# Kernel tuning notes

Measured on AMD Instinct MI355X. Metric: run time of the kernel, lower is better.

The kernel has to match this reference:

```python
import jax, jax.numpy as jnp
import numpy as np

D = 256; DFFN = 1024; H = 8; NLVL = 4; NPNT = 4; HD = D // H
BS = 4; NQ = 100; NPTS = 25
SPATIAL = [(128, 128), (64, 64), (32, 32), (16, 16)]
LEN_IN = sum(h * w for h, w in SPATIAL)


def _ln(x, g, b, eps=1e-5):
    m = x.mean(-1, keepdims=True)
    v = ((x - m) ** 2).mean(-1, keepdims=True)
    return (x - m) * jax.lax.rsqrt(v + eps) * g + b


def _mha(q, k, v, w_in, b_in, w_out, b_out):
    # torch nn.MultiheadAttention math, batch-first layout [B,S,D]
    B, Sq, _ = q.shape; Sk = k.shape[1]
    wq, wk, wv = jnp.split(w_in, 3, 0); bq, bk, bv = jnp.split(b_in, 3)
    qh = (q @ wq.T + bq).reshape(B, Sq, H, HD).transpose(0, 2, 1, 3)
    kh = (k @ wk.T + bk).reshape(B, Sk, H, HD).transpose(0, 2, 1, 3)
    vh = (v @ wv.T + bv).reshape(B, Sk, H, HD).transpose(0, 2, 1, 3)
    a = jax.nn.softmax(jnp.einsum('bhqd,bhkd->bhqk', qh, kh) * (1.0 / float(np.sqrt(HD))), -1)
    o = jnp.einsum('bhqk,bhkd->bhqd', a, vh).transpose(0, 2, 1, 3).reshape(B, Sq, D)
    return o @ w_out.T + b_out


def _msdeform(query, ref, src, off_w, off_b, aw_w, aw_b, val_w, val_b, out_w, out_b):
    # MSDeformAttn: per-query multi-level bilinear sampling + weighted aggregation
    bs, Lq, _ = query.shape
    value = (src @ val_w.T + val_b).reshape(bs, LEN_IN, H, HD)
    off = (query @ off_w.T + off_b).reshape(bs, Lq, H, NLVL, NPNT, 2)
    aw = jax.nn.softmax((query @ aw_w.T + aw_b).reshape(bs, Lq, H, NLVL * NPNT), -1)
    aw = aw.reshape(bs, Lq, H, NLVL, NPNT)
    norm = jnp.array([[w, h] for h, w in SPATIAL], jnp.float32)  # (W,H) per level
    loc = ref[:, :, None, :, None, :] + off / norm[None, None, None, :, None, :]
    out = jnp.zeros((bs, H, Lq, HD), query.dtype)
    start = 0
    for l, (hh, ww) in enumerate(SPATIAL):
        v_l = value[:, start:start + hh * ww].transpose(0, 2, 1, 3)  # [bs,H,hw,HD]
        start += hh * ww
        # grid_sample align_corners=False pixel coords: loc*size - 0.5
        x = (loc[:, :, :, l, :, 0] * ww - 0.5).transpose(0, 2, 1, 3).reshape(bs, H, Lq * NPNT)
        y = (loc[:, :, :, l, :, 1] * hh - 0.5).transpose(0, 2, 1, 3).reshape(bs, H, Lq * NPNT)
        x0 = jnp.floor(x); y0 = jnp.floor(y); wx = x - x0; wy = y - y0
        x0i = x0.astype(jnp.int32); y0i = y0.astype(jnp.int32); x1i = x0i + 1; y1i = y0i + 1
        def g(xi, yi):
            valid = ((xi >= 0) & (xi < ww) & (yi >= 0) & (yi < hh)).astype(query.dtype)
            idx = jnp.clip(yi, 0, hh - 1) * ww + jnp.clip(xi, 0, ww - 1)
            return jnp.take_along_axis(v_l, idx[..., None], axis=2) * valid[..., None]
        s = (g(x0i, y0i) * ((1 - wx) * (1 - wy))[..., None]
             + g(x1i, y0i) * (wx * (1 - wy))[..., None]
             + g(x0i, y1i) * ((1 - wx) * wy)[..., None]
             + g(x1i, y1i) * (wx * wy)[..., None])
        s = s.reshape(bs, H, Lq, NPNT, HD)
        out = out + (s * aw[:, :, :, l].transpose(0, 2, 1, 3)[..., None]).sum(3)
    return out.transpose(0, 2, 1, 3).reshape(bs, Lq, D) @ out_w.T + out_b


def _fwd(tgt, query_pos, reference_points, src,
         w_in_intra, b_in_intra, w_out_intra, b_out_intra, g_norm_intra, b_norm_intra,
         w_in_inter, b_in_inter, w_out_inter, b_out_inter, g_norm_inter, b_norm_inter,
         off_w, off_b, aw_w, aw_b, val_w, val_b, co_w, co_b, g_norm_cross, b_norm_cross,
         lin1_w, lin1_b, lin2_w, lin2_b, g_norm3, b_norm3):
    bs, nq, npts, d = tgt.shape
    # intra-instance self-attention (over control points)
    q = (tgt + query_pos).reshape(bs * nq, npts, d)
    t2 = _mha(q, q, tgt.reshape(bs * nq, npts, d), w_in_intra, b_in_intra, w_out_intra, b_out_intra)
    tgt = _ln(tgt + t2.reshape(bs, nq, npts, d), g_norm_intra, b_norm_intra)
    # inter-instance self-attention (over queries), no pos embed per source code
    ti = tgt.transpose(0, 2, 1, 3).reshape(bs * npts, nq, d)
    t2 = _mha(ti, ti, ti, w_in_inter, b_in_inter, w_out_inter, b_out_inter)
    ti = _ln(ti + t2, g_norm_inter, b_norm_inter).reshape(bs, npts, nq, d).transpose(0, 2, 1, 3)
    # deformable cross-attention
    ref = jnp.broadcast_to(reference_points[:, :, None], (bs, nq, npts, NLVL, 2)).reshape(bs, nq * npts, NLVL, 2)
    qc = (ti + query_pos).reshape(bs, nq * npts, d)
    t2 = _msdeform(qc, ref, src, off_w, off_b, aw_w, aw_b, val_w, val_b, co_w, co_b).reshape(bs, nq, npts, d)
    tgt = _ln(ti + t2, g_norm_cross, b_norm_cross)
    # FFN
    ff = jax.nn.relu(tgt @ lin1_w.T + lin1_b) @ lin2_w.T + lin2_b
    return _ln(tgt + ff, g_norm3, b_norm3)


def setup_inputs() -> dict:
    key = jax.random.key(0)
    ki = iter(jax.random.split(key, 40))
    def rn(shape, sc=0.02):
        return jax.random.normal(next(ki), shape, jnp.float32) * sc
    inp = dict(
        tgt=jax.random.normal(next(ki), (BS, NQ, NPTS, D), jnp.float32),
        query_pos=jax.random.normal(next(ki), (BS, NQ, NPTS, D), jnp.float32),
        reference_points=jax.random.uniform(next(ki), (BS, NQ, NLVL, 2), jnp.float32),
        src=jax.random.normal(next(ki), (BS, LEN_IN, D), jnp.float32),
        w_in_intra=rn((3 * D, D)), b_in_intra=jnp.zeros((3 * D,), jnp.float32),
        w_out_intra=rn((D, D)), b_out_intra=jnp.zeros((D,), jnp.float32),
        g_norm_intra=jnp.ones((D,), jnp.float32), b_norm_intra=jnp.zeros((D,), jnp.float32),
        w_in_inter=rn((3 * D, D)), b_in_inter=jnp.zeros((3 * D,), jnp.float32),
        w_out_inter=rn((D, D)), b_out_inter=jnp.zeros((D,), jnp.float32),
        g_norm_inter=jnp.ones((D,), jnp.float32), b_norm_inter=jnp.zeros((D,), jnp.float32),
        off_w=rn((H * NLVL * NPNT * 2, D), 0.001), off_b=rn((H * NLVL * NPNT * 2,), 0.5),
        aw_w=rn((H * NLVL * NPNT, D)), aw_b=jnp.zeros((H * NLVL * NPNT,), jnp.float32),
        val_w=rn((D, D)), val_b=jnp.zeros((D,), jnp.float32),
        co_w=rn((D, D)), co_b=jnp.zeros((D,), jnp.float32),
        g_norm_cross=jnp.ones((D,), jnp.float32), b_norm_cross=jnp.zeros((D,), jnp.float32),
        lin1_w=rn((DFFN, D)), lin1_b=jnp.zeros((DFFN,), jnp.float32),
        lin2_w=rn((D, DFFN)), lin2_b=jnp.zeros((D,), jnp.float32),
        g_norm3=jnp.ones((D,), jnp.float32), b_norm3=jnp.zeros((D,), jnp.float32),
        src_spatial_shapes=jnp.array(SPATIAL, jnp.int32),
        level_start_index=jnp.array(np.cumsum([0] + [h * w for h, w in SPATIAL[:-1]]), jnp.int32),
    )
    return inp


def reference(tgt, query_pos, reference_points, src,
              w_in_intra, b_in_intra, w_out_intra, b_out_intra, g_norm_intra, b_norm_intra,
              w_in_inter, b_in_inter, w_out_inter, b_out_inter, g_norm_inter, b_norm_inter,
              off_w, off_b, aw_w, aw_b, val_w, val_b, co_w, co_b, g_norm_cross, b_norm_cross,
              lin1_w, lin1_b, lin2_w, lin2_b, g_norm3, b_norm3,
              src_spatial_shapes, level_start_index):
    # spatial shapes / level starts are compile-time constants (SPATIAL); args kept for signature parity
    return _fwd(tgt, query_pos, reference_points, src,
                w_in_intra, b_in_intra, w_out_intra, b_out_intra, g_norm_intra, b_norm_intra,
                w_in_inter, b_in_inter, w_out_inter, b_out_inter, g_norm_inter, b_norm_inter,
                off_w, off_b, aw_w, aw_b, val_w, val_b, co_w, co_b, g_norm_cross, b_norm_cross,
                lin1_w, lin1_b, lin2_w, lin2_b, g_norm3, b_norm3)
```

## Files before the change

kernel.cpp:

```cpp
#include <hip/hip_runtime.h>
#include <math.h>

#define DMODEL 256
#define HEADS  8
#define HDIM   32
#define BS     4
#define NQ     100
#define NPTS   25
#define LQ     2500
#define M10K   10000
#define LEN_IN 21760
#define MVAL   87040

typedef float f32x4 __attribute__((ext_vector_type(4)));
typedef short s16x8 __attribute__((ext_vector_type(8)));
typedef unsigned short u16;

static __device__ __forceinline__ short f2bf(float f) {
    unsigned u = __builtin_bit_cast(unsigned, f);
    u = (u + 0x7fffu + ((u >> 16) & 1u)) >> 16;
    return (short)u;
}
static __device__ __forceinline__ unsigned pack2(float lo, float hi) {
    return (unsigned)(u16)f2bf(lo) | ((unsigned)(u16)f2bf(hi) << 16);
}
static __device__ __forceinline__ float bf_lo(unsigned u) {
    return __builtin_bit_cast(float, u << 16);
}
static __device__ __forceinline__ float bf_hi(unsigned u) {
    return __builtin_bit_cast(float, u & 0xffff0000u);
}

#define LDSK   40
#define LDSK64 72

__global__ __launch_bounds__(256) void convert_weights_kernel(
    const float* __restrict__ s0, const float* __restrict__ s1,
    const float* __restrict__ s2, const float* __restrict__ s3,
    const float* __restrict__ s4, const float* __restrict__ s5,
    const float* __restrict__ s6, const float* __restrict__ s7,
    const float* __restrict__ s8, const float* __restrict__ s9,
    u16* __restrict__ dst)
{
    int t8 = (blockIdx.x * 256 + threadIdx.x) * 8;
    if (t8 >= 1277952) return;
    const float* s; int base;
    if      (t8 <  196608) { s = s0; base = 0;       }
    else if (t8 <  262144) { s = s1; base = 196608;  }
    else if (t8 <  458752) { s = s2; base = 262144;  }
    else if (t8 <  524288) { s = s3; base = 458752;  }
    else if (t8 <  589824) { s = s4; base = 524288;  }
    else if (t8 <  622592) { s = s5; base = 589824;  }
    else if (t8 <  688128) { s = s6; base = 622592;  }
    else if (t8 <  753664) { s = s7; base = 688128;  }
    else if (t8 < 1015808) { s = s8; base = 753664;  }
    else                   { s = s9; base = 1015808; }
    const float* p = s + (t8 - base);
    float4 a = *(const float4*)p;
    float4 b = *(const float4*)(p + 4);
    s16x8 v;
    v[0]=f2bf(a.x); v[1]=f2bf(a.y); v[2]=f2bf(a.z); v[3]=f2bf(a.w);
    v[4]=f2bf(b.x); v[5]=f2bf(b.y); v[6]=f2bf(b.z); v[7]=f2bf(b.w);
    *(s16x8*)(dst + t8) = v;
}

__global__ __launch_bounds__(256) void add_convert_kernel(
    const float* __restrict__ a, const float* __restrict__ b,
    u16* __restrict__ xb, u16* __restrict__ ab, int n8)
{
    int i = blockIdx.x * 256 + threadIdx.x;
    if (i >= n8) return;
    size_t o = (size_t)i * 8;
    float4 a0 = *(const float4*)(a + o);
    float4 a1 = *(const float4*)(a + o + 4);
    if (ab) {
        s16x8 v;
        v[0]=f2bf(a0.x); v[1]=f2bf(a0.y); v[2]=f2bf(a0.z); v[3]=f2bf(a0.w);
        v[4]=f2bf(a1.x); v[5]=f2bf(a1.y); v[6]=f2bf(a1.z); v[7]=f2bf(a1.w);
        *(s16x8*)(ab + o) = v;
    }
    if (b) {
        float4 b0 = *(const float4*)(b + o);
        float4 b1 = *(const float4*)(b + o + 4);
        a0.x += b0.x; a0.y += b0.y; a0.z += b0.z; a0.w += b0.w;
        a1.x += b1.x; a1.y += b1.y; a1.z += b1.z; a1.w += b1.w;
    }
    s16x8 v;
    v[0]=f2bf(a0.x); v[1]=f2bf(a0.y); v[2]=f2bf(a0.z); v[3]=f2bf(a0.w);
    v[4]=f2bf(a1.x); v[5]=f2bf(a1.y); v[6]=f2bf(a1.z); v[7]=f2bf(a1.w);
    *(s16x8*)(xb + o) = v;
}

__global__ __launch_bounds__(256) void gemm_mfma_kernel(
    const u16* __restrict__ A, int lda,
    const u16* __restrict__ W, int K,
    const float* __restrict__ bias,
    void* __restrict__ Cv, int ldc,
    int M, int relu, int out_bf16)
{
    __shared__ short As[64 * LDSK64];
    __shared__ short Ws[64 * LDSK64];

    const int tid = threadIdx.x;
    const int m0 = blockIdx.y * 64, n0 = blockIdx.x * 64;
    const int srow = tid >> 2;
    const int sk = (tid & 3) * 16;
    const int wave = tid >> 6;
    const int wm = wave & 1, wn = wave >> 1;
    const int lane = tid & 63;
    const int lrow = lane & 15;
    const int kq = lane >> 4;

    const int gm = m0 + srow;
    const u16* aptr = A + (size_t)gm * lda + sk;
    const u16* wptr = W + (size_t)(n0 + srow) * K + sk;

    f32x4 acc[2][2];
#pragma unroll
    for (int i = 0; i < 2; ++i)
#pragma unroll
        for (int j = 0; j < 2; ++j) acc[i][j] = (f32x4)(0.f);

    s16x8 a0 = (s16x8)0, a1 = (s16x8)0, w0, w1;
    if (gm < M) { a0 = *(const s16x8*)aptr; a1 = *(const s16x8*)(aptr + 8); }
    w0 = *(const s16x8*)wptr; w1 = *(const s16x8*)(wptr + 8);

    for (int k0 = 0; k0 < K; k0 += 64) {
        *(s16x8*)&As[srow * LDSK64 + sk]     = a0;
        *(s16x8*)&As[srow * LDSK64 + sk + 8] = a1;
        *(s16x8*)&Ws[srow * LDSK64 + sk]     = w0;
        *(s16x8*)&Ws[srow * LDSK64 + sk + 8] = w1;
        __syncthreads();
        if (k0 + 64 < K) {
            if (gm < M) {
                a0 = *(const s16x8*)(aptr + k0 + 64);
                a1 = *(const s16x8*)(aptr + k0 + 72);
            }
            w0 = *(const s16x8*)(wptr + k0 + 64);
            w1 = *(const s16x8*)(wptr + k0 + 72);
        }

#pragma unroll
        for (int s = 0; s < 2; ++s) {
            s16x8 af[2], bfv[2];
#pragma unroll
            for (int i = 0; i < 2; ++i)
                af[i] = *(const s16x8*)&As[(wm * 32 + i * 16 + lrow) * LDSK64 + s * 32 + kq * 8];
#pragma unroll
            for (int j = 0; j < 2; ++j)
                bfv[j] = *(const s16x8*)&Ws[(wn * 32 + j * 16 + lrow) * LDSK64 + s * 32 + kq * 8];
#pragma unroll
            for (int i = 0; i < 2; ++i)
#pragma unroll
                for (int j = 0; j < 2; ++j)
                    acc[i][j] = __builtin_amdgcn_mfma_f32_16x16x32_bf16(af[i], bfv[j], acc[i][j], 0, 0, 0);
        }
        __syncthreads();
    }

#pragma unroll
    for (int i = 0; i < 2; ++i)
#pragma unroll
        for (int j = 0; j < 2; ++j) {
            int col = n0 + wn * 32 + j * 16 + lrow;
            float bv = bias[col];
#pragma unroll
            for (int reg = 0; reg < 4; ++reg) {
                int gmo = m0 + wm * 32 + i * 16 + kq * 4 + reg;
                if (gmo < M) {
                    float v = acc[i][j][reg] + bv;
                    if (relu) v = fmaxf(v, 0.f);
                    if (out_bf16)
                        ((u16*)Cv)[(size_t)gmo * ldc + col] = (u16)f2bf(v);
                    else
                        ((float*)Cv)[(size_t)gmo * ldc + col] = v;
                }
            }
        }
}

__global__ __launch_bounds__(256) void gemm_mfma128_kernel(
    const u16* __restrict__ A, int lda,
    const u16* __restrict__ W, int K,
    const float* __restrict__ bias,
    void* __restrict__ Cv, int ldc,
    int M, int relu, int out_bf16)
{
    __shared__ short As[128 * LDSK];
    __shared__ short Ws[128 * LDSK];

    const int tid = threadIdx.x;
    const int m0 = blockIdx.y * 128, n0 = blockIdx.x * 128;

    const int srow = tid >> 1;
    const int sk = (tid & 1) * 16;

    const int wave = tid >> 6;
    const int wm = wave & 1, wn = wave >> 1;
    const int lane = tid & 63;
    const int lrow = lane & 15;
    const int kq = lane >> 4;

    const int gm = m0 + srow;
    const u16* aptr = A + (size_t)gm * lda + sk;
    const u16* wptr = W + (size_t)(n0 + srow) * K + sk;

    f32x4 acc[4][4];
#pragma unroll
    for (int i = 0; i < 4; ++i)
#pragma unroll
        for (int j = 0; j < 4; ++j) acc[i][j] = (f32x4)(0.f);

    s16x8 a0 = (s16x8)0, a1 = (s16x8)0, w0, w1;
    if (gm < M) { a0 = *(const s16x8*)aptr; a1 = *(const s16x8*)(aptr + 8); }
    w0 = *(const s16x8*)wptr; w1 = *(const s16x8*)(wptr + 8);

    for (int k0 = 0; k0 < K; k0 += 32) {
        *(s16x8*)&As[srow * LDSK + sk]     = a0;
        *(s16x8*)&As[srow * LDSK + sk + 8] = a1;
        *(s16x8*)&Ws[srow * LDSK + sk]     = w0;
        *(s16x8*)&Ws[srow * LDSK + sk + 8] = w1;
        __syncthreads();
        if (k0 + 32 < K) {
            if (gm < M) {
                a0 = *(const s16x8*)(aptr + k0 + 32);
                a1 = *(const s16x8*)(aptr + k0 + 40);
            }
            w0 = *(const s16x8*)(wptr + k0 + 32);
            w1 = *(const s16x8*)(wptr + k0 + 40);
        }

        s16x8 af[4], bfv[4];
#pragma unroll
        for (int i = 0; i < 4; ++i)
            af[i] = *(const s16x8*)&As[(wm * 64 + i * 16 + lrow) * LDSK + kq * 8];
#pragma unroll
        for (int j = 0; j < 4; ++j)
            bfv[j] = *(const s16x8*)&Ws[(wn * 64 + j * 16 + lrow) * LDSK + kq * 8];
#pragma unroll
        for (int i = 0; i < 4; ++i)
#pragma unroll
            for (int j = 0; j < 4; ++j)
                acc[i][j] = __builtin_amdgcn_mfma_f32_16x16x32_bf16(af[i], bfv[j], acc[i][j], 0, 0, 0);
        __syncthreads();
    }

#pragma unroll
    for (int i = 0; i < 4; ++i)
#pragma unroll
        for (int j = 0; j < 4; ++j) {
            int col = n0 + wn * 64 + j * 16 + lrow;
            float bv = bias[col];
#pragma unroll
            for (int reg = 0; reg < 4; ++reg) {
                int gmo = m0 + wm * 64 + i * 16 + kq * 4 + reg;
                if (gmo < M) {
                    float v = acc[i][j][reg] + bv;
                    if (relu) v = fmaxf(v, 0.f);
                    if (out_bf16)
                        ((u16*)Cv)[(size_t)gmo * ldc + col] = (u16)f2bf(v);
                    else
                        ((float*)Cv)[(size_t)gmo * ldc + col] = v;
                }
            }
        }
}

__global__ __launch_bounds__(256) void gemm_value64_kernel(
    const float* __restrict__ A,
    const u16* __restrict__ W,
    const float* __restrict__ bias,
    u16* __restrict__ C)
{
    __shared__ short As[64 * LDSK];
    __shared__ short Ws[128 * LDSK];

    const int tid = threadIdx.x;
    const int n0 = blockIdx.x * 128;
    const int m0 = blockIdx.y * 64;

    const int arow = tid >> 2;
    const int ak = (tid & 3) * 8;
    const int wrow = tid >> 1;
    const int wk = (tid & 1) * 16;

    const float* aptr = A + (size_t)(m0 + arow) * 256 + ak;
    const u16* wptr = W + (size_t)(n0 + wrow) * 256 + wk;

    const int wave = tid >> 6;
    const int wm = wave & 1, wn = wave >> 1;
    const int lane = tid & 63;
    const int lrow = lane & 15, kq = lane >> 4;

    f32x4 acc[2][4];
#pragma unroll
    for (int i = 0; i < 2; ++i)
#pragma unroll
        for (int j = 0; j < 4; ++j) acc[i][j] = (f32x4)(0.f);

    float4 pa0 = *(const float4*)aptr;
    float4 pa1 = *(const float4*)(aptr + 4);
    s16x8 w0 = *(const s16x8*)wptr;
    s16x8 w1 = *(const s16x8*)(wptr + 8);

    for (int k0 = 0; k0 < 256; k0 += 32) {
        s16x8 av;
        av[0]=f2bf(pa0.x); av[1]=f2bf(pa0.y); av[2]=f2bf(pa0.z); av[3]=f2bf(pa0.w);
        av[4]=f2bf(pa1.x); av[5]=f2bf(pa1.y); av[6]=f2bf(pa1.z); av[7]=f2bf(pa1.w);
        *(s16x8*)&As[arow * LDSK + ak]     = av;
        *(s16x8*)&Ws[wrow * LDSK + wk]     = w0;
        *(s16x8*)&Ws[wrow * LDSK + wk + 8] = w1;
        __syncthreads();
        if (k0 + 32 < 256) {
            pa0 = *(const float4*)(aptr + k0 + 32);
            pa1 = *(const float4*)(aptr + k0 + 36);
            w0 = *(const s16x8*)(wptr + k0 + 32);
            w1 = *(const s16x8*)(wptr + k0 + 40);
        }

        s16x8 af[2], bfv[4];
#pragma unroll
        for (int i = 0; i < 2; ++i)
            af[i] = *(const s16x8*)&As[(wm * 32 + i * 16 + lrow) * LDSK + kq * 8];
#pragma unroll
        for (int j = 0; j < 4; ++j)
            bfv[j] = *(const s16x8*)&Ws[(wn * 64 + j * 16 + lrow) * LDSK + kq * 8];
#pragma unroll
        for (int i = 0; i < 2; ++i)
#pragma unroll
            for (int j = 0; j < 4; ++j)
                acc[i][j] = __builtin_amdgcn_mfma_f32_16x16x32_bf16(af[i], bfv[j], acc[i][j], 0, 0, 0);
        __syncthreads();
    }

#pragma unroll
    for (int i = 0; i < 2; ++i)
#pragma unroll
        for (int j = 0; j < 4; ++j) {
            int col = n0 + wn * 64 + j * 16 + lrow;
            float bv = bias[col];
#pragma unroll
            for (int reg = 0; reg < 4; ++reg) {
                int gmo = m0 + wm * 32 + i * 16 + kq * 4 + reg;
                C[(size_t)gmo * 256 + col] = (u16)f2bf(acc[i][j][reg] + bv);
            }
        }
}

__global__ __launch_bounds__(256) void inter_attn_mfma_kernel(
    const float* __restrict__ qkv, u16* __restrict__ out, float scale)
{
    __shared__ __align__(16) u16 Qs[112 * 40];
    __shared__ __align__(16) u16 Ks[112 * 40];
    __shared__ __align__(16) u16 Vt[32 * 136];
    __shared__ __align__(16) u16 Ps[112 * 136];

    const int b = blockIdx.x, h = blockIdx.y;
    const float* base = qkv + (size_t)b * 100 * 768;
    const int tid = threadIdx.x;
    const int wave = tid >> 6, lane = tid & 63;
    const int lr = lane & 15, quad = lane >> 4;

    for (int i = tid; i < 12 * 20; i += 256) {
        int row = 100 + i / 20, c = (i % 20) * 2;
        *(unsigned*)&Qs[row * 40 + c] = 0;
        *(unsigned*)&Ks[row * 40 + c] = 0;
    }
    for (int i = tid; i < 2176; i += 256) ((unsigned*)Vt)[i] = 0;
    for (int i = tid; i < 7616; i += 256) ((unsigned*)Ps)[i] = 0;
    __syncthreads();

    for (int idx = tid; idx < 2400; idx += 256) {
        int row = idx / 24, s = idx % 24;
        const float* p = (s < 8)  ? base + row * 768 + h * 32 + s * 4
                       : (s < 16) ? base + row * 768 + 256 + h * 32 + (s - 8) * 4
                                  : base + row * 768 + 512 + h * 32 + (s - 16) * 4;
        float4 f = *(const float4*)p;
        if (s < 8) {
            unsigned* q = (unsigned*)&Qs[row * 40 + s * 4];
            q[0] = pack2(f.x, f.y); q[1] = pack2(f.z, f.w);
        } else if (s < 16) {
            unsigned* q = (unsigned*)&Ks[row * 40 + (s - 8) * 4];
            q[0] = pack2(f.x, f.y); q[1] = pack2(f.z, f.w);
        } else {
            int d0 = (s - 16) * 4;
            Vt[(d0 + 0) * 136 + row] = (u16)f2bf(f.x);
            Vt[(d0 + 1) * 136 + row] = (u16)f2bf(f.y);
            Vt[(d0 + 2) * 136 + row] = (u16)f2bf(f.z);
            Vt[(d0 + 3) * 136 + row] = (u16)f2bf(f.w);
        }
    }
    __syncthreads();

#pragma unroll 1
    for (int rr = 0; rr < 2; ++rr) {
        int rt = wave + rr * 4;
        if (rt < 7) {
            s16x8 aq = *(const s16x8*)&Qs[(rt * 16 + lr) * 40 + quad * 8];
            f32x4 sc[7];
#pragma unroll
            for (int ct = 0; ct < 7; ++ct) {
                s16x8 bk = *(const s16x8*)&Ks[(ct * 16 + lr) * 40 + quad * 8];
                sc[ct] = __builtin_amdgcn_mfma_f32_16x16x32_bf16(aq, bk, (f32x4)(0.f), 0, 0, 0);
            }
            const bool colok[7] = {true, true, true, true, true, true, (lr < 4)};
#pragma unroll
            for (int reg = 0; reg < 4; ++reg) {
                float mx = -1e30f;
#pragma unroll
                for (int ct = 0; ct < 7; ++ct) {
                    float sv = sc[ct][reg] * scale;
                    sc[ct][reg] = sv;
                    if (colok[ct]) mx = fmaxf(mx, sv);
                }
#pragma unroll
                for (int d = 1; d < 16; d <<= 1) mx = fmaxf(mx, __shfl_xor(mx, d));
                float ssum = 0.f;
#pragma unroll
                for (int ct = 0; ct < 7; ++ct) {
                    float pv = colok[ct] ? __expf(sc[ct][reg] - mx) : 0.f;
                    sc[ct][reg] = pv;
                    ssum += pv;
                }
#pragma unroll
                for (int d = 1; d < 16; d <<= 1) ssum += __shfl_xor(ssum, d);
                float inv = 1.f / ssum;
                int prow = rt * 16 + quad * 4 + reg;
#pragma unroll
                for (int ct = 0; ct < 7; ++ct)
                    Ps[prow * 136 + ct * 16 + lr] = (u16)f2bf(sc[ct][reg] * inv);
            }
        }
    }
    __syncthreads();

#pragma unroll 1
    for (int rr = 0; rr < 2; ++rr) {
        int rt = wave + rr * 4;
        if (rt < 7) {
            f32x4 o0 = (f32x4)(0.f), o1 = (f32x4)(0.f);
#pragma unroll
            for (int kk = 0; kk < 4; ++kk) {
                s16x8 ap = *(const s16x8*)&Ps[(rt * 16 + lr) * 136 + kk * 32 + quad * 8];
                s16x8 bv0 = *(const s16x8*)&Vt[lr * 136 + kk * 32 + quad * 8];
                s16x8 bv1 = *(const s16x8*)&Vt[(16 + lr) * 136 + kk * 32 + quad * 8];
                o0 = __builtin_amdgcn_mfma_f32_16x16x32_bf16(ap, bv0, o0, 0, 0, 0);
                o1 = __builtin_amdgcn_mfma_f32_16x16x32_bf16(ap, bv1, o1, 0, 0, 0);
            }
#pragma unroll
            for (int reg = 0; reg < 4; ++reg) {
                int q = rt * 16 + quad * 4 + reg;
                if (q < 100) {
                    u16* op = out + ((size_t)b * 100 + q) * 256 + h * 32;
                    op[lr]      = (u16)f2bf(o0[reg]);
                    op[16 + lr] = (u16)f2bf(o1[reg]);
                }
            }
        }
    }
}

__global__ __launch_bounds__(256) void intra_attn_kernel(
    const float* __restrict__ qkv, u16* __restrict__ out, float scale)
{
    __shared__ float4 KV[25][128];

    const int b = blockIdx.x;
    const int h = threadIdx.x >> 5, r = threadIdx.x & 31;
    const float* base = qkv + (size_t)b * 25 * 768;

    for (int idx = threadIdx.x; idx < 3200; idx += 256) {
        int row = idx >> 7, c = idx & 127;
        KV[row][c] = *(const float4*)(base + row * 768 + 256 + c * 4);
    }

    float q[32];
    if (r < 25) {
        const float* qp = base + r * 768 + h * 32;
#pragma unroll
        for (int c4 = 0; c4 < 8; ++c4) {
            float4 f = *(const float4*)(qp + c4 * 4);
            q[c4*4+0] = f.x; q[c4*4+1] = f.y; q[c4*4+2] = f.z; q[c4*4+3] = f.w;
        }
    }
    __syncthreads();

    if (r < 25) {
        float m = -1e30f, l = 0.f, acc[32];
#pragma unroll
        for (int c = 0; c < 32; ++c) acc[c] = 0.f;
#pragma unroll 2
        for (int j = 0; j < 25; ++j) {
            const float4* kr = &KV[j][h * 8];
            float dot = 0.f;
#pragma unroll
            for (int c4 = 0; c4 < 8; ++c4) {
                float4 kf = kr[c4];
                dot = fmaf(q[c4*4+0], kf.x, dot);
                dot = fmaf(q[c4*4+1], kf.y, dot);
                dot = fmaf(q[c4*4+2], kf.z, dot);
                dot = fmaf(q[c4*4+3], kf.w, dot);
            }
            dot *= scale;
            float mn = fmaxf(m, dot);
            float alpha = __expf(m - mn);
            float p = __expf(dot - mn);
            l = l * alpha + p;
            const float4* vr = &KV[j][64 + h * 8];
#pragma unroll
            for (int c4 = 0; c4 < 8; ++c4) {
                float4 vf = vr[c4];
                acc[c4*4+0] = acc[c4*4+0] * alpha + p * vf.x;
                acc[c4*4+1] = acc[c4*4+1] * alpha + p * vf.y;
                acc[c4*4+2] = acc[c4*4+2] * alpha + p * vf.z;
                acc[c4*4+3] = acc[c4*4+3] * alpha + p * vf.w;
            }
            m = mn;
        }
        float inv = 1.f / l;
        unsigned* op = (unsigned*)(out + ((size_t)b * 25 + r) * 256 + h * 32);
#pragma unroll
        for (int c = 0; c < 16; ++c)
            op[c] = pack2(acc[2*c] * inv, acc[2*c+1] * inv);
    }
}

__global__ __launch_bounds__(64) void add_ln_kernel(
    const float* __restrict__ a, const float* __restrict__ b,
    const float* __restrict__ g, const float* __restrict__ beta,
    float* __restrict__ out, u16* __restrict__ out_bf, int transpose_mode)
{
    const int r = blockIdx.x;
    const int lane = threadIdx.x;
    const float* ar = a + (size_t)r * 256;
    const float* br = b + (size_t)r * 256;
    float x[4];
    float s = 0.f;
#pragma unroll
    for (int i = 0; i < 4; ++i) {
        x[i] = ar[lane + 64 * i] + br[lane + 64 * i];
        s += x[i];
    }
#pragma unroll
    for (int off = 32; off >= 1; off >>= 1) s += __shfl_xor(s, off);
    float mean = s * (1.f / 256.f);
    float vs = 0.f;
#pragma unroll
    for (int i = 0; i < 4; ++i) { float d = x[i] - mean; vs += d * d; }
#pragma unroll
    for (int off = 32; off >= 1; off >>= 1) vs += __shfl_xor(vs, off);
    float rstd = rsqrtf(vs * (1.f / 256.f) + 1e-5f);

    size_t ro = r;
    if (transpose_mode) {
        int q = r % 100; int bp = r / 100; int p = bp % 25; int bb = bp / 25;
        ro = ((size_t)bb * 100 + q) * 25 + p;
    }
    float* orow = out + ro * 256;
    u16* brow = out_bf ? out_bf + ro * 256 : (u16*)0;
#pragma unroll
    for (int i = 0; i < 4; ++i) {
        int c = lane + 64 * i;
        float v = (x[i] - mean) * rstd * g[c] + beta[c];
        orow[c] = v;
        if (brow) brow[c] = (u16)f2bf(v);
    }
}

__global__ __launch_bounds__(64) void tgt_to_ti_kernel(
    const float* __restrict__ tgt1, float* __restrict__ ti, u16* __restrict__ tib)
{
    const int r = blockIdx.x;
    int q = r % 100; int bp = r / 100; int p = bp % 25; int b = bp / 25;
    const float4* srcp = (const float4*)(tgt1 + (((size_t)b * 100 + q) * 25 + p) * 256);
    float4 v = srcp[threadIdx.x];
    ((float4*)(ti + (size_t)r * 256))[threadIdx.x] = v;
    uint2 pk = make_uint2(pack2(v.x, v.y), pack2(v.z, v.w));
    ((uint2*)(tib + (size_t)r * 256))[threadIdx.x] = pk;
}

__global__ __launch_bounds__(256, 4) void msdeform_sample_kernel(
    const u16* __restrict__ value,
    const float* __restrict__ off,
    const float* __restrict__ awl,
    const float* __restrict__ refp,
    u16* __restrict__ sampled)
{
    const int unit = blockIdx.x * 8 + (threadIdx.x >> 5);
    const int t = threadIdx.x & 31;
    const int h = t >> 2, c8 = t & 3;
    const int b = unit / LQ, lq = unit - b * LQ;
    const int q = lq / NPTS;

    const float* awp = awl + (size_t)unit * 128 + h * 16;
    float w[16];
    float mx = -1e30f;
#pragma unroll
    for (int k = 0; k < 16; ++k) { w[k] = awp[k]; mx = fmaxf(mx, w[k]); }
    float sum = 0.f;
#pragma unroll
    for (int k = 0; k < 16; ++k) { w[k] = __expf(w[k] - mx); sum += w[k]; }
    const float inv = 1.f / sum;

    const float* offp = off + (size_t)unit * 256 + h * 32;
    const float* rp = refp + ((size_t)b * 100 + q) * 8;
    const u16* vbase = value + (size_t)b * LEN_IN * 256 + h * 32 + c8 * 8;

    float acc[8];
#pragma unroll
    for (int k = 0; k < 8; ++k) acc[k] = 0.f;

    int start = 0;
    const int sz[4] = {128, 64, 32, 16};
#pragma unroll
    for (int l = 0; l < 4; ++l) {
        const int hh = sz[l], ww = sz[l];
        const float rx = rp[l * 2 + 0], ry = rp[l * 2 + 1];
#pragma unroll 1
        for (int pt = 0; pt < 4; ++pt) {
            float ox = offp[(l * 4 + pt) * 2 + 0];
            float oy = offp[(l * 4 + pt) * 2 + 1];
            float x = rx * ww + ox - 0.5f;
            float y = ry * hh + oy - 0.5f;
            float x0f = floorf(x), y0f = floorf(y);
            float wx = x - x0f, wy = y - y0f;
            int x0 = (int)x0f, y0 = (int)y0f;
            int x1 = x0 + 1, y1 = y0 + 1;
            float aw = w[l * 4 + pt] * inv;

            int x0c = min(max(x0, 0), ww - 1), x1c = min(max(x1, 0), ww - 1);
            int y0c = min(max(y0, 0), hh - 1), y1c = min(max(y1, 0), hh - 1);
            float w00 = aw * (1.f - wx) * (1.f - wy);
            float w10 = aw * wx * (1.f - wy);
            float w01 = aw * (1.f - wx) * wy;
            float w11 = aw * wx * wy;
            if (!(x0 >= 0 && x0 < ww)) { w00 = 0.f; w01 = 0.f; }
            if (!(x1 >= 0 && x1 < ww)) { w10 = 0.f; w11 = 0.f; }
            if (!(y0 >= 0 && y0 < hh)) { w00 = 0.f; w10 = 0.f; }
            if (!(y1 >= 0 && y1 < hh)) { w01 = 0.f; w11 = 0.f; }

            uint4 u00 = *(const uint4*)(vbase + (size_t)(start + y0c * ww + x0c) * 256);
            uint4 u10 = *(const uint4*)(vbase + (size_t)(start + y0c * ww + x1c) * 256);
            uint4 u01 = *(const uint4*)(vbase + (size_t)(start + y1c * ww + x0c) * 256);
            uint4 u11 = *(const uint4*)(vbase + (size_t)(start + y1c * ww + x1c) * 256);

#define ACC4(u, wgt) \
            acc[0] = fmaf(wgt, bf_lo(u.x), acc[0]); \
            acc[1] = fmaf(wgt, bf_hi(u.x), acc[1]); \
            acc[2] = fmaf(wgt, bf_lo(u.y), acc[2]); \
            acc[3] = fmaf(wgt, bf_hi(u.y), acc[3]); \
            acc[4] = fmaf(wgt, bf_lo(u.z), acc[4]); \
            acc[5] = fmaf(wgt, bf_hi(u.z), acc[5]); \
            acc[6] = fmaf(wgt, bf_lo(u.w), acc[6]); \
            acc[7] = fmaf(wgt, bf_hi(u.w), acc[7]);
            ACC4(u00, w00); ACC4(u10, w10); ACC4(u01, w01); ACC4(u11, w11);
#undef ACC4
        }
        start += hh * ww;
    }

    uint4 pk;
    pk.x = pack2(acc[0], acc[1]); pk.y = pack2(acc[2], acc[3]);
    pk.z = pack2(acc[4], acc[5]); pk.w = pack2(acc[6], acc[7]);
    *(uint4*)(sampled + (size_t)unit * 256 + h * 32 + c8 * 8) = pk;
}

extern "C" void kernel_launch(void* const* d_in, const int* in_sizes, int n_in,
                              void* d_out, int out_size, void* d_ws, size_t ws_size,
                              hipStream_t stream)
{
    (void)in_sizes; (void)n_in; (void)out_size; (void)ws_size;

    const float* tgt        = (const float*)d_in[0];
    const float* query_pos  = (const float*)d_in[1];
    const float* refp       = (const float*)d_in[2];
    const float* src        = (const float*)d_in[3];
    const float* w_in_intra = (const float*)d_in[4];
    const float* b_in_intra = (const float*)d_in[5];
    const float* w_out_intra= (const float*)d_in[6];
    const float* b_out_intra= (const float*)d_in[7];
    const float* g_ln_intra = (const float*)d_in[8];
    const float* b_ln_intra = (const float*)d_in[9];
    const float* w_in_inter = (const float*)d_in[10];
    const float* b_in_inter = (const float*)d_in[11];
    const float* w_out_inter= (const float*)d_in[12];
    const float* b_out_inter= (const float*)d_in[13];
    const float* g_ln_inter = (const float*)d_in[14];
    const float* b_ln_inter = (const float*)d_in[15];
    const float* off_w      = (const float*)d_in[16];
    const float* off_b      = (const float*)d_in[17];
    const float* aw_w       = (const float*)d_in[18];
    const float* aw_b       = (const float*)d_in[19];
    const float* val_w      = (const float*)d_in[20];
    const float* val_b      = (const float*)d_in[21];
    const float* co_w       = (const float*)d_in[22];
    const float* co_b       = (const float*)d_in[23];
    const float* g_ln_cross = (const float*)d_in[24];
    const float* b_ln_cross = (const float*)d_in[25];
    const float* lin1_w     = (const float*)d_in[26];
    const float* lin1_b     = (const float*)d_in[27];
    const float* lin2_w     = (const float*)d_in[28];
    const float* lin2_b     = (const float*)d_in[29];
    const float* g_ln3      = (const float*)d_in[30];
    const float* b_ln3      = (const float*)d_in[31];

    float* ws    = (float*)d_ws;
    float* qkv   = ws;
    float* tmp   = ws + 7680000;
    u16*   attnb = (u16*)(ws + 10240000);
    float* tgt1  = ws + 11520000;
    float* ti    = ws + 14080000;
    u16*   tib   = (u16*)(ws + 16640000);
    float* tA    = ws + 17920000;
    u16*   qcb   = (u16*)(ws + 20480000);
    u16*   x1b   = (u16*)(ws + 21760000);
    u16*   tgtb  = (u16*)(ws + 23040000);
    float* awl   = ws + 24320000;
    u16*   valueb= (u16*)(ws + 25600000);
    u16*   wb    = (u16*)(ws + 36741120);
    float* out   = (float*)d_out;

    u16* wb_in_intra  = wb;
    u16* wb_out_intra = wb + 196608;
    u16* wb_in_inter  = wb + 262144;
    u16* wb_out_inter = wb + 458752;
    u16* wb_off       = wb + 524288;
    u16* wb_aw        = wb + 589824;
    u16* wb_val       = wb + 622592;
    u16* wb_co        = wb + 688128;
    u16* wb_lin1      = wb + 753664;
    u16* wb_lin2      = wb + 1015808;

    const float scale = 0.17677669529663687f;
    const int MB64  = (M10K + 63) / 64;
    const int MB128 = (M10K + 127) / 128;

    convert_weights_kernel<<<624, 256, 0, stream>>>(
        w_in_intra, w_out_intra, w_in_inter, w_out_inter, off_w,
        aw_w, val_w, co_w, lin1_w, lin2_w, wb);
    add_convert_kernel<<<1250, 256, 0, stream>>>(tgt, query_pos, x1b, tgtb, 320000);

    gemm_mfma128_kernel<<<dim3(4, MB128), 256, 0, stream>>>(x1b, 256, wb_in_intra, 256,
                                                            b_in_intra, qkv, 768, M10K, 0, 0);
    gemm_mfma_kernel<<<dim3(4, MB64), 256, 0, stream>>>(tgtb, 256, wb_in_intra + 512 * 256, 256,
                                                        b_in_intra + 512, qkv + 512, 768, M10K, 0, 0);
    intra_attn_kernel<<<400, 256, 0, stream>>>(qkv, attnb, scale);
    gemm_mfma_kernel<<<dim3(4, MB64), 256, 0, stream>>>(attnb, 256, wb_out_intra, 256,
                                                        b_out_intra, tmp, 256, M10K, 0, 0);
    add_ln_kernel<<<M10K, 64, 0, stream>>>(tgt, tmp, g_ln_intra, b_ln_intra, tgt1, (u16*)0, 0);

    tgt_to_ti_kernel<<<M10K, 64, 0, stream>>>(tgt1, ti, tib);
    gemm_mfma128_kernel<<<dim3(6, MB128), 256, 0, stream>>>(tib, 256, wb_in_inter, 256,
                                                            b_in_inter, qkv, 768, M10K, 0, 0);
    inter_attn_mfma_kernel<<<dim3(100, 8), 256, 0, stream>>>(qkv, attnb, scale);
    gemm_mfma_kernel<<<dim3(4, MB64), 256, 0, stream>>>(attnb, 256, wb_out_inter, 256,
                                                        b_out_inter, tmp, 256, M10K, 0, 0);
    add_ln_kernel<<<M10K, 64, 0, stream>>>(ti, tmp, g_ln_inter, b_ln_inter, tA, (u16*)0, 1);

    add_convert_kernel<<<1250, 256, 0, stream>>>(tA, query_pos, qcb, (u16*)0, 320000);
    gemm_value64_kernel<<<dim3(2, 1360), 256, 0, stream>>>(src, wb_val, val_b, valueb);
    gemm_mfma_kernel<<<dim3(4, MB64), 256, 0, stream>>>(qcb, 256, wb_off, 256,
                                                        off_b, tgt1, 256, M10K, 0, 0);
    gemm_mfma_kernel<<<dim3(2, MB64), 256, 0, stream>>>(qcb, 256, wb_aw, 256,
                                                        aw_b, awl, 128, M10K, 0, 0);
    msdeform_sample_kernel<<<1250, 256, 0, stream>>>(valueb, tgt1, awl, refp, attnb);
    gemm_mfma_kernel<<<dim3(4, MB64), 256, 0, stream>>>(attnb, 256, wb_co, 256,
                                                        co_b, tmp, 256, M10K, 0, 0);
    add_ln_kernel<<<M10K, 64, 0, stream>>>(tA, tmp, g_ln_cross, b_ln_cross, ti, tib, 0);

    gemm_mfma128_kernel<<<dim3(8, MB128), 256, 0, stream>>>(tib, 256, wb_lin1, 256,
                                                            lin1_b, valueb, 1024, M10K, 1, 1);
    gemm_mfma_kernel<<<dim3(4, MB64), 256, 0, stream>>>(valueb, 1024, wb_lin2, 1024,
                                                        lin2_b, tmp, 256, M10K, 0, 0);
    add_ln_kernel<<<M10K, 64, 0, stream>>>(ti, tmp, g_ln3, b_ln3, out, (u16*)0, 0);
}
```

Baseline: 469.3 us.

## Rewrite value-projection GEMM with direct global-to-LDS async loads and 4-stage pipeline

```diff
diff --git a/kernel.cpp b/kernel.cpp
--- a/kernel.cpp
+++ b/kernel.cpp
@@ -15,6 +15,9 @@
 typedef float f32x4 __attribute__((ext_vector_type(4)));
 typedef short s16x8 __attribute__((ext_vector_type(8)));
 typedef unsigned short u16;
+
+#define AS1 __attribute__((address_space(1)))
+#define AS3 __attribute__((address_space(3)))
 
 static __device__ __forceinline__ short f2bf(float f) {
     unsigned u = __builtin_bit_cast(unsigned, f);
@@ -266,82 +269,100 @@
         }
 }
 
-__global__ __launch_bounds__(256) void gemm_value64_kernel(
+__global__ __launch_bounds__(256) void gemm_value_gll_kernel(
     const float* __restrict__ A,
     const u16* __restrict__ W,
     const float* __restrict__ bias,
     u16* __restrict__ C)
 {
-    __shared__ short As[64 * LDSK];
-    __shared__ short Ws[128 * LDSK];
+    __shared__ __align__(16) short Wp[64 * 264];
+    __shared__ __align__(16) float Abuf[4][64 * 32];
 
     const int tid = threadIdx.x;
-    const int n0 = blockIdx.x * 128;
+    const int n0 = blockIdx.x * 64;
     const int m0 = blockIdx.y * 64;
-
-    const int arow = tid >> 2;
-    const int ak = (tid & 3) * 8;
-    const int wrow = tid >> 1;
-    const int wk = (tid & 1) * 16;
-
-    const float* aptr = A + (size_t)(m0 + arow) * 256 + ak;
-    const u16* wptr = W + (size_t)(n0 + wrow) * 256 + wk;
-
-    const int wave = tid >> 6;
+    const int wave = tid >> 6, lane = tid & 63;
+    const int lrow = lane & 15, kq = lane >> 4;
     const int wm = wave & 1, wn = wave >> 1;
-    const int lane = tid & 63;
-    const int lrow = lane & 15, kq = lane >> 4;
-
-    f32x4 acc[2][4];
+
+    {
+        const int row = tid >> 2, cb = (tid & 3) * 64;
+        const u16* src = W + (size_t)(n0 + row) * 256 + cb;
+        short* dst = &Wp[row * 264 + cb];
+#pragma unroll
+        for (int i = 0; i < 8; ++i)
+            *(s16x8*)(dst + i * 8) = *(const s16x8*)(src + i * 8);
+    }
+
+    const int r0 = tid >> 3,         l0 = (tid & 7) ^ (r0 & 7);
+    const int r1 = (tid + 256) >> 3, l1 = (tid & 7) ^ (r1 & 7);
+    const float* g0 = A + (size_t)(m0 + r0) * 256 + l0 * 4;
+    const float* g1 = A + (size_t)(m0 + r1) * 256 + l1 * 4;
+
+#define STAGE_A(tt) do {                                                     \
+    float* d0_ = &Abuf[(tt) & 3][wave * 256];                                \
+    float* d1_ = &Abuf[(tt) & 3][1024 + wave * 256];                         \
+    __builtin_amdgcn_global_load_lds(                                        \
+        (const AS1 unsigned*)(g0 + (tt) * 32), (AS3 unsigned*)d0_, 16, 0, 0);\
+    __builtin_amdgcn_global_load_lds(                                        \
+        (const AS1 unsigned*)(g1 + (tt) * 32), (AS3 unsigned*)d1_, 16, 0, 0);\
+} while (0)
+
+    STAGE_A(0);
+    STAGE_A(1);
+    asm volatile("s_waitcnt lgkmcnt(0)" ::: "memory");
+    __builtin_amdgcn_sched_barrier(0);
+    __builtin_amdgcn_s_barrier();
+
+    f32x4 acc[2][2];
 #pragma unroll
     for (int i = 0; i < 2; ++i)
 #pragma unroll
-        for (int j = 0; j < 4; ++j) acc[i][j] = (f32x4)(0.f);
-
-    float4 pa0 = *(const float4*)aptr;
-    float4 pa1 = *(const float4*)(aptr + 4);
-    s16x8 w0 = *(const s16x8*)wptr;
-    s16x8 w1 = *(const s16x8*)(wptr + 8);
-
-    for (int k0 = 0; k0 < 256; k0 += 32) {
-        s16x8 av;
-        av[0]=f2bf(pa0.x); av[1]=f2bf(pa0.y); av[2]=f2bf(pa0.z); av[3]=f2bf(pa0.w);
-        av[4]=f2bf(pa1.x); av[5]=f2bf(pa1.y); av[6]=f2bf(pa1.z); av[7]=f2bf(pa1.w);
-        *(s16x8*)&As[arow * LDSK + ak]     = av;
-        *(s16x8*)&Ws[wrow * LDSK + wk]     = w0;
-        *(s16x8*)&Ws[wrow * LDSK + wk + 8] = w1;
-        __syncthreads();
-        if (k0 + 32 < 256) {
-            pa0 = *(const float4*)(aptr + k0 + 32);
-            pa1 = *(const float4*)(aptr + k0 + 36);
-            w0 = *(const s16x8*)(wptr + k0 + 32);
-            w1 = *(const s16x8*)(wptr + k0 + 40);
-        }
-
-        s16x8 af[2], bfv[4];
+        for (int j = 0; j < 2; ++j) acc[i][j] = (f32x4)(0.f);
+
+#pragma unroll
+    for (int t = 0; t < 8; ++t) {
+        if (t < 6) STAGE_A(t + 2);
+        if (t < 6)       asm volatile("s_waitcnt vmcnt(4)" ::: "memory");
+        else if (t == 6) asm volatile("s_waitcnt vmcnt(2)" ::: "memory");
+        else             asm volatile("s_waitcnt vmcnt(0)" ::: "memory");
+        __builtin_amdgcn_sched_barrier(0);
+        __builtin_amdgcn_s_barrier();
+
+        const float* ab = Abuf[t & 3];
+        s16x8 af[2];
+#pragma unroll
+        for (int i = 0; i < 2; ++i) {
+            const int row = wm * 32 + i * 16 + lrow;
+            const int sw = row & 7;
+            const float4 f0 = *(const float4*)&ab[row * 32 + (((kq << 1) | 0) ^ sw) * 4];
+            const float4 f1 = *(const float4*)&ab[row * 32 + (((kq << 1) | 1) ^ sw) * 4];
+            af[i][0] = f2bf(f0.x); af[i][1] = f2bf(f0.y);
+            af[i][2] = f2bf(f0.z); af[i][3] = f2bf(f0.w);
+            af[i][4] = f2bf(f1.x); af[i][5] = f2bf(f1.y);
+            af[i][6] = f2bf(f1.z); af[i][7] = f2bf(f1.w);
+        }
+        s16x8 bfv[2];
+#pragma unroll
+        for (int j = 0; j < 2; ++j)
+            bfv[j] = *(const s16x8*)&Wp[(wn * 32 + j * 16 + lrow) * 264 + t * 32 + kq * 8];
 #pragma unroll
         for (int i = 0; i < 2; ++i)
-            af[i] = *(const s16x8*)&As[(wm * 32 + i * 16 + lrow) * LDSK + kq * 8];
-#pragma unroll
-        for (int j = 0; j < 4; ++j)
-            bfv[j] = *(const s16x8*)&Ws[(wn * 64 + j * 16 + lrow) * LDSK + kq * 8];
-#pragma unroll
-        for (int i = 0; i < 2; ++i)
-#pragma unroll
-            for (int j = 0; j < 4; ++j)
+#pragma unroll
+            for (int j = 0; j < 2; ++j)
                 acc[i][j] = __builtin_amdgcn_mfma_f32_16x16x32_bf16(af[i], bfv[j], acc[i][j], 0, 0, 0);
-        __syncthreads();
-    }
+    }
+#undef STAGE_A
 
 #pragma unroll
     for (int i = 0; i < 2; ++i)
 #pragma unroll
-        for (int j = 0; j < 4; ++j) {
-            int col = n0 + wn * 64 + j * 16 + lrow;
-            float bv = bias[col];
+        for (int j = 0; j < 2; ++j) {
+            const int col = n0 + wn * 32 + j * 16 + lrow;
+            const float bv = bias[col];
 #pragma unroll
             for (int reg = 0; reg < 4; ++reg) {
-                int gmo = m0 + wm * 32 + i * 16 + kq * 4 + reg;
+                const int gmo = m0 + wm * 32 + i * 16 + kq * 4 + reg;
                 C[(size_t)gmo * 256 + col] = (u16)f2bf(acc[i][j][reg] + bv);
             }
         }
@@ -758,7 +779,7 @@
     add_ln_kernel<<<M10K, 64, 0, stream>>>(ti, tmp, g_ln_inter, b_ln_inter, tA, (u16*)0, 1);
 
     add_convert_kernel<<<1250, 256, 0, stream>>>(tA, query_pos, qcb, (u16*)0, 320000);
-    gemm_value64_kernel<<<dim3(2, 1360), 256, 0, stream>>>(src, wb_val, val_b, valueb);
+    gemm_value_gll_kernel<<<dim3(4, 1360), 256, 0, stream>>>(src, wb_val, val_b, valueb);
     gemm_mfma_kernel<<<dim3(4, MB64), 256, 0, stream>>>(qcb, 256, wb_off, 256,
                                                         off_b, tgt1, 256, M10K, 0, 0);
     gemm_mfma_kernel<<<dim3(2, MB64), 256, 0, stream>>>(qcb, 256, wb_aw, 256,
```

Result: slower. 504.9 us (+7.6%).

## Fuse intra LayerNorm with inter-layout transpose and emit bf16 inter QKV

Applied to the files above, without the earlier changes.

```diff
diff --git a/kernel.cpp b/kernel.cpp
--- a/kernel.cpp
+++ b/kernel.cpp
@@ -348,7 +348,7 @@
 }
 
 __global__ __launch_bounds__(256) void inter_attn_mfma_kernel(
-    const float* __restrict__ qkv, u16* __restrict__ out, float scale)
+    const u16* __restrict__ qkv, u16* __restrict__ out, float scale)
 {
     __shared__ __align__(16) u16 Qs[112 * 40];
     __shared__ __align__(16) u16 Ks[112 * 40];
@@ -356,7 +356,7 @@
     __shared__ __align__(16) u16 Ps[112 * 136];
 
     const int b = blockIdx.x, h = blockIdx.y;
-    const float* base = qkv + (size_t)b * 100 * 768;
+    const u16* base = qkv + (size_t)b * 100 * 768;
     const int tid = threadIdx.x;
     const int wave = tid >> 6, lane = tid & 63;
     const int lr = lane & 15, quad = lane >> 4;
@@ -372,22 +372,19 @@
 
     for (int idx = tid; idx < 2400; idx += 256) {
         int row = idx / 24, s = idx % 24;
-        const float* p = (s < 8)  ? base + row * 768 + h * 32 + s * 4
-                       : (s < 16) ? base + row * 768 + 256 + h * 32 + (s - 8) * 4
-                                  : base + row * 768 + 512 + h * 32 + (s - 16) * 4;
-        float4 f = *(const float4*)p;
+        const u16* p = (s < 8)  ? base + row * 768 + h * 32 + s * 4
+                     : (s < 16) ? base + row * 768 + 256 + h * 32 + (s - 8) * 4
+                                : base + row * 768 + 512 + h * 32 + (s - 16) * 4;
         if (s < 8) {
-            unsigned* q = (unsigned*)&Qs[row * 40 + s * 4];
-            q[0] = pack2(f.x, f.y); q[1] = pack2(f.z, f.w);
+            *(uint2*)&Qs[row * 40 + s * 4] = *(const uint2*)p;
         } else if (s < 16) {
-            unsigned* q = (unsigned*)&Ks[row * 40 + (s - 8) * 4];
-            q[0] = pack2(f.x, f.y); q[1] = pack2(f.z, f.w);
+            *(uint2*)&Ks[row * 40 + (s - 8) * 4] = *(const uint2*)p;
         } else {
             int d0 = (s - 16) * 4;
-            Vt[(d0 + 0) * 136 + row] = (u16)f2bf(f.x);
-            Vt[(d0 + 1) * 136 + row] = (u16)f2bf(f.y);
-            Vt[(d0 + 2) * 136 + row] = (u16)f2bf(f.z);
-            Vt[(d0 + 3) * 136 + row] = (u16)f2bf(f.w);
+            Vt[(d0 + 0) * 136 + row] = p[0];
+            Vt[(d0 + 1) * 136 + row] = p[1];
+            Vt[(d0 + 2) * 136 + row] = p[2];
+            Vt[(d0 + 3) * 136 + row] = p[3];
         }
     }
     __syncthreads();
@@ -552,9 +549,12 @@
     float rstd = rsqrtf(vs * (1.f / 256.f) + 1e-5f);
 
     size_t ro = r;
-    if (transpose_mode) {
+    if (transpose_mode == 1) {
         int q = r % 100; int bp = r / 100; int p = bp % 25; int bb = bp / 25;
         ro = ((size_t)bb * 100 + q) * 25 + p;
+    } else if (transpose_mode == 2) {
+        int p = r % 25; int t = r / 25; int q = t % 100; int bb = t / 100;
+        ro = ((size_t)bb * 25 + p) * 100 + q;
     }
     float* orow = out + ro * 256;
     u16* brow = out_bf ? out_bf + ro * 256 : (u16*)0;
@@ -565,18 +565,6 @@
         orow[c] = v;
         if (brow) brow[c] = (u16)f2bf(v);
     }
-}
-
-__global__ __launch_bounds__(64) void tgt_to_ti_kernel(
-    const float* __restrict__ tgt1, float* __restrict__ ti, u16* __restrict__ tib)
-{
-    const int r = blockIdx.x;
-    int q = r % 100; int bp = r / 100; int p = bp % 25; int b = bp / 25;
-    const float4* srcp = (const float4*)(tgt1 + (((size_t)b * 100 + q) * 25 + p) * 256);
-    float4 v = srcp[threadIdx.x];
-    ((float4*)(ti + (size_t)r * 256))[threadIdx.x] = v;
-    uint2 pk = make_uint2(pack2(v.x, v.y), pack2(v.z, v.w));
-    ((uint2*)(tib + (size_t)r * 256))[threadIdx.x] = pk;
 }
 
 __global__ __launch_bounds__(256, 4) void msdeform_sample_kernel(
@@ -720,6 +708,8 @@
     u16*   wb    = (u16*)(ws + 36741120);
     float* out   = (float*)d_out;
 
+    u16* qkvb = (u16*)qkv;
+
     u16* wb_in_intra  = wb;
     u16* wb_out_intra = wb + 196608;
     u16* wb_in_inter  = wb + 262144;
@@ -747,12 +737,11 @@
     intra_attn_kernel<<<400, 256, 0, stream>>>(qkv, attnb, scale);
     gemm_mfma_kernel<<<dim3(4, MB64), 256, 0, stream>>>(attnb, 256, wb_out_intra, 256,
                                                         b_out_intra, tmp, 256, M10K, 0, 0);
-    add_ln_kernel<<<M10K, 64, 0, stream>>>(tgt, tmp, g_ln_intra, b_ln_intra, tgt1, (u16*)0, 0);
-
-    tgt_to_ti_kernel<<<M10K, 64, 0, stream>>>(tgt1, ti, tib);
+    add_ln_kernel<<<M10K, 64, 0, stream>>>(tgt, tmp, g_ln_intra, b_ln_intra, ti, tib, 2);
+
     gemm_mfma128_kernel<<<dim3(6, MB128), 256, 0, stream>>>(tib, 256, wb_in_inter, 256,
-                                                            b_in_inter, qkv, 768, M10K, 0, 0);
-    inter_attn_mfma_kernel<<<dim3(100, 8), 256, 0, stream>>>(qkv, attnb, scale);
+                                                            b_in_inter, qkvb, 768, M10K, 0, 1);
+    inter_attn_mfma_kernel<<<dim3(100, 8), 256, 0, stream>>>(qkvb, attnb, scale);
     gemm_mfma_kernel<<<dim3(4, MB64), 256, 0, stream>>>(attnb, 256, wb_out_inter, 256,
                                                         b_out_inter, tmp, 256, M10K, 0, 0);
     add_ln_kernel<<<M10K, 64, 0, stream>>>(ti, tmp, g_ln_inter, b_ln_inter, tA, (u16*)0, 1);
```

Result: slower. 479.2 us (+2.1%).
